# Performance work log

Hardware: AMD Instinct MI355X
Metric: run time of the kernel (lower is better)

The kernel has to match this reference:

```python
import jax, jax.numpy as jnp
import numpy as np

N, E = 20000, 320000
IN_F, H, D = 1280, 4, 128
HD = H * D  # 512
NEG_SLOPE = 0.2


def setup_inputs() -> dict:
    key = jax.random.key(0)
    ks = jax.random.split(key, 16)
    feature = jax.random.normal(ks[0], (1, N, IN_F), dtype=jnp.float32)
    src = jax.random.randint(ks[1], (E,), 0, N, dtype=jnp.int32)
    dst = jnp.sort(jax.random.randint(ks[2], (E,), 0, N, dtype=jnp.int32))
    s1 = 1.0 / np.sqrt(IN_F)
    s2 = 1.0 / np.sqrt(HD)
    W1 = jax.random.normal(ks[3], (IN_F, HD), dtype=jnp.float32) * s1
    al1 = jax.random.normal(ks[4], (H, D), dtype=jnp.float32) * s2
    ar1 = jax.random.normal(ks[5], (H, D), dtype=jnp.float32) * s2
    b1 = jnp.zeros((HD,), dtype=jnp.float32)
    W2 = jax.random.normal(ks[6], (HD, HD), dtype=jnp.float32) * s2
    al2 = jax.random.normal(ks[7], (H, D), dtype=jnp.float32) * s2
    ar2 = jax.random.normal(ks[8], (H, D), dtype=jnp.float32) * s2
    b2 = jnp.zeros((HD,), dtype=jnp.float32)
    Wfc = jax.random.normal(ks[9], (HD, 64), dtype=jnp.float32) * s2
    bfc = jnp.zeros((64,), dtype=jnp.float32)
    return dict(feature=feature, src=src, dst=dst, W1=W1, al1=al1, ar1=ar1,
                b1=b1, W2=W2, al2=al2, ar2=ar2, b2=b2, Wfc=Wfc, bfc=bfc)


def gat_conv(x, src, dst, W, al, ar, b):
    # x: (N, F_in) -> (N, H, D). DGL GATConv math, negative_slope=0.2.
    h = (x @ W).reshape(N, H, D)
    el = jnp.sum(h * al, axis=-1)                       # (N, H)
    er = jnp.sum(h * ar, axis=-1)                       # (N, H)
    e = jax.nn.leaky_relu(el[src] + er[dst], NEG_SLOPE)  # (E, H)
    # edge softmax segmented by destination node
    m = jax.ops.segment_max(e, dst, num_segments=N, indices_are_sorted=True)
    ex = jnp.exp(e - m[dst])                            # (E, H)
    denom = jax.ops.segment_sum(ex, dst, num_segments=N, indices_are_sorted=True)
    alpha = ex / denom[dst]                             # (E, H)
    out = jax.ops.segment_sum(alpha[:, :, None] * h[src], dst,
                              num_segments=N, indices_are_sorted=True)  # (N,H,D)
    return out + b.reshape(H, D)


def reference(feature, src, dst, W1, al1, ar1, b1, W2, al2, ar2, b2, Wfc, bfc):
    x = feature[0]                                      # squeeze(0) -> (N, 1280)
    out = gat_conv(x, src, dst, W1, al1, ar1, b1)
    out = jax.nn.elu(out).reshape(N, HD)
    out = gat_conv(out, src, dst, W2, al2, ar2, b2)
    out = jax.nn.elu(out).reshape(N, HD)
    out = out @ Wfc + bfc                               # (N, 64)
    out = jax.nn.elu(out[None])                         # (1, N, 64)
    return out
```

## Files before the change

### kernel.cpp

```cpp
#include <hip/hip_runtime.h>
#include <hip/hip_bf16.h>
#include <math.h>

typedef __bf16 bf16_t;
typedef __bf16 bf16x8 __attribute__((ext_vector_type(8)));
typedef float f32x4 __attribute__((ext_vector_type(4)));

__device__ __forceinline__ void gload_lds16(const void* g, void* l) {
  __builtin_amdgcn_global_load_lds((const __attribute__((address_space(1))) void*)g,
                                   (__attribute__((address_space(3))) void*)l, 16, 0, 0);
}

__global__ void castk(const float* __restrict__ in, bf16_t* __restrict__ out, int n) {
  int i = (blockIdx.x * blockDim.x + threadIdx.x) * 8;
  if (i >= n) return;
  float4 a = *(const float4*)(in + i);
  float4 b = *(const float4*)(in + i + 4);
  bf16x8 o;
  o[0] = (bf16_t)a.x; o[1] = (bf16_t)a.y; o[2] = (bf16_t)a.z; o[3] = (bf16_t)a.w;
  o[4] = (bf16_t)b.x; o[5] = (bf16_t)b.y; o[6] = (bf16_t)b.z; o[7] = (bf16_t)b.w;
  *(bf16x8*)(out + i) = o;
}

__global__ void transk(const float* __restrict__ in, bf16_t* __restrict__ out,
                       int K, int N) {
  __shared__ float t[32][33];
  int n0 = blockIdx.x * 32, k0 = blockIdx.y * 32;
  int tx = threadIdx.x & 31, ty = threadIdx.x >> 5;
#pragma unroll
  for (int r = ty; r < 32; r += 8) t[r][tx] = in[(size_t)(k0 + r) * N + n0 + tx];
  __syncthreads();
#pragma unroll
  for (int r = ty; r < 32; r += 8)
    out[(size_t)(n0 + r) * K + k0 + tx] = (bf16_t)t[tx][r];
}

__global__ void rowoffk(const int* __restrict__ dst, int* __restrict__ ro, int N, int E) {
  int n = blockIdx.x * blockDim.x + threadIdx.x;
  if (n > N) return;
  if (n == N) { ro[N] = E; return; }
  int lo = 0, hi = E;
  while (lo < hi) { int mid = (lo + hi) >> 1; if (dst[mid] < n) lo = mid + 1; else hi = mid; }
  ro[n] = lo;
}

__global__ void elerk(const bf16_t* __restrict__ Hb, const float* __restrict__ al,
                      const float* __restrict__ ar, float* __restrict__ el,
                      float* __restrict__ er, int N) {
  int node = blockIdx.x * 4 + (threadIdx.x >> 6);
  int lane = threadIdx.x & 63;
  if (node >= N) return;
  bf16x8 v = *(const bf16x8*)(Hb + (size_t)node * 512 + lane * 8);
  int head = lane >> 4;
  int dbase = (lane & 15) * 8;
  float sl = 0.f, sr = 0.f;
#pragma unroll
  for (int t = 0; t < 8; t++) {
    float f = (float)v[t];
    sl += f * al[head * 128 + dbase + t];
    sr += f * ar[head * 128 + dbase + t];
  }
#pragma unroll
  for (int off = 1; off < 16; off <<= 1) {
    sl += __shfl_xor(sl, off);
    sr += __shfl_xor(sr, off);
  }
  if ((lane & 15) == 0) {
    el[node * 4 + head] = sl;
    er[node * 4 + head] = sr;
  }
}

__global__ void edgek(const float* __restrict__ el, const float* __restrict__ er,
                      const int* __restrict__ src, const int* __restrict__ dst,
                      float* __restrict__ pw, int E) {
  int e = blockIdx.x * blockDim.x + threadIdx.x;
  if (e >= E) return;
  int s = src[e], d = dst[e];
  float4 ev = *(const float4*)(el + (size_t)s * 4);
  float4 rv = *(const float4*)(er + (size_t)d * 4);
  float c;
  c = ev.x + rv.x; c = c >= 0.f ? c : 0.2f * c; pw[e] = __expf(c);
  c = ev.y + rv.y; c = c >= 0.f ? c : 0.2f * c; pw[(size_t)E + e] = __expf(c);
  c = ev.z + rv.z; c = c >= 0.f ? c : 0.2f * c; pw[(size_t)2 * E + e] = __expf(c);
  c = ev.w + rv.w; c = c >= 0.f ? c : 0.2f * c; pw[(size_t)3 * E + e] = __expf(c);
}

#define GK_NPB 32
__global__ __launch_bounds__(256) void gatherk(
    const bf16_t* __restrict__ Hb, const float* __restrict__ pw,
    const int* __restrict__ src, const int* __restrict__ ro,
    const float* __restrict__ bias, bf16_t* __restrict__ out, int N, int E) {
  const int slice = blockIdx.x & 7;
  const int group = blockIdx.x >> 3;
  const int w = threadIdx.x >> 6, lane = threadIdx.x & 63;
  const int g = lane >> 3;
  const int oct = lane & 7;
  const int head = slice >> 1;
  const float* __restrict__ ph = pw + (size_t)head * E;
  const int dimbase = slice * 64 + oct * 8;

  const int n = group * GK_NPB + w * 8 + g;
  const int e0 = ro[n], e1 = ro[n + 1];

  float acc[8] = {0.f, 0.f, 0.f, 0.f, 0.f, 0.f, 0.f, 0.f};
  float psum = 0.f;

  for (int e = e0; e < e1; e++) {
    const int s = src[e];
    const float pp = ph[e];
    const bf16x8 v = *(const bf16x8*)(Hb + (size_t)s * 512 + dimbase);
    psum += pp;
#pragma unroll
    for (int t = 0; t < 8; t++) acc[t] += pp * (float)v[t];
  }

  const float ih = psum > 0.f ? 1.0f / psum : 0.f;
  const float4 b0 = *(const float4*)(bias + dimbase);
  const float4 b1 = *(const float4*)(bias + dimbase + 4);
  bf16x8 o; float vv;
  vv = acc[0] * ih + b0.x; o[0] = (bf16_t)(vv > 0.f ? vv : expm1f(vv));
  vv = acc[1] * ih + b0.y; o[1] = (bf16_t)(vv > 0.f ? vv : expm1f(vv));
  vv = acc[2] * ih + b0.z; o[2] = (bf16_t)(vv > 0.f ? vv : expm1f(vv));
  vv = acc[3] * ih + b0.w; o[3] = (bf16_t)(vv > 0.f ? vv : expm1f(vv));
  vv = acc[4] * ih + b1.x; o[4] = (bf16_t)(vv > 0.f ? vv : expm1f(vv));
  vv = acc[5] * ih + b1.y; o[5] = (bf16_t)(vv > 0.f ? vv : expm1f(vv));
  vv = acc[6] * ih + b1.z; o[6] = (bf16_t)(vv > 0.f ? vv : expm1f(vv));
  vv = acc[7] * ih + b1.w; o[7] = (bf16_t)(vv > 0.f ? vv : expm1f(vv));
  *(bf16x8*)(out + (size_t)n * 512 + dimbase) = o;
}

template <int BN, int WM, int WN, int EPI>
__global__ __launch_bounds__(256) void gemm_bt(
    const bf16_t* __restrict__ A, const bf16_t* __restrict__ Bt,
    void* __restrict__ C, const float* __restrict__ bias,
    int M, int N, int K) {
  constexpr int BM = 128, BK = 32;
  constexpr int WTM = BM / WM, WTN = BN / WN;
  constexpr int MF = WTM / 16, NF = WTN / 16;

  __shared__ bf16_t sA[BM][BK];
  __shared__ bf16_t sB[BN][BK];

  const int tid = threadIdx.x;
  const int wid = tid >> 6, lane = tid & 63;
  const int wr = wid / WN, wc = wid % WN;

  const int nby = N / BN;
  const int nwg = gridDim.x;
  const int q = nwg >> 3, r = nwg & 7;
  const int xcd = blockIdx.x & 7, pos = blockIdx.x >> 3;
  const int wg = (xcd < r ? xcd * (q + 1) : r * (q + 1) + (xcd - r) * q) + pos;
  const int row0 = (wg / nby) * BM;
  const int col0 = (wg % nby) * BN;

  f32x4 acc[MF][NF];
#pragma unroll
  for (int i = 0; i < MF; i++)
#pragma unroll
    for (int j = 0; j < NF; j++) acc[i][j] = (f32x4){0.f, 0.f, 0.f, 0.f};

  const int lr = lane >> 2;
  const int lkb = (lane & 3) * 8;

  for (int k0 = 0; k0 < K; k0 += BK) {
#pragma unroll
    for (int i = 0; i < BM / 16; i += 4) {
      int r2 = (i + wid) * 16 + lr;
      int grow = row0 + r2; if (grow > M - 1) grow = M - 1;
      gload_lds16(A + (size_t)grow * K + k0 + lkb, &sA[(i + wid) * 16][0]);
    }
#pragma unroll
    for (int i = 0; i < BN / 16; i += 4) {
      int r2 = (i + wid) * 16 + lr;
      gload_lds16(Bt + (size_t)(col0 + r2) * K + k0 + lkb, &sB[(i + wid) * 16][0]);
    }
    __syncthreads();
    bf16x8 af[MF], bfr[NF];
#pragma unroll
    for (int i = 0; i < MF; i++)
      af[i] = *(const bf16x8*)&sA[wr * WTM + i * 16 + (lane & 15)][(lane >> 4) * 8];
#pragma unroll
    for (int j = 0; j < NF; j++)
      bfr[j] = *(const bf16x8*)&sB[wc * WTN + j * 16 + (lane & 15)][(lane >> 4) * 8];
#pragma unroll
    for (int i = 0; i < MF; i++)
#pragma unroll
      for (int j = 0; j < NF; j++)
        acc[i][j] = __builtin_amdgcn_mfma_f32_16x16x32_bf16(af[i], bfr[j], acc[i][j], 0, 0, 0);
    __syncthreads();
  }

#pragma unroll
  for (int i = 0; i < MF; i++) {
#pragma unroll
    for (int j = 0; j < NF; j++) {
#pragma unroll
      for (int rr = 0; rr < 4; rr++) {
        int row = row0 + wr * WTM + i * 16 + (lane >> 4) * 4 + rr;
        int col = col0 + wc * WTN + j * 16 + (lane & 15);
        if (row < M) {
          float v = acc[i][j][rr];
          if constexpr (EPI == 0) {
            ((bf16_t*)C)[(size_t)row * N + col] = (bf16_t)v;
          } else {
            v += bias[col];
            v = v > 0.f ? v : expm1f(v);
            ((float*)C)[(size_t)row * N + col] = v;
          }
        }
      }
    }
  }
}

extern "C" void kernel_launch(void* const* d_in, const int* in_sizes, int n_in,
                              void* d_out, int out_size, void* d_ws, size_t ws_size,
                              hipStream_t stream) {
  const float* feature = (const float*)d_in[0];
  const int* src = (const int*)d_in[1];
  const int* dst = (const int*)d_in[2];
  const float* W1 = (const float*)d_in[3];
  const float* al1 = (const float*)d_in[4];
  const float* ar1 = (const float*)d_in[5];
  const float* b1 = (const float*)d_in[6];
  const float* W2 = (const float*)d_in[7];
  const float* al2 = (const float*)d_in[8];
  const float* ar2 = (const float*)d_in[9];
  const float* b2 = (const float*)d_in[10];
  const float* Wfc = (const float*)d_in[11];
  const float* bfc = (const float*)d_in[12];

  const int N = 20000, E = 320000, INF = 1280, HD = 512;

  char* ws = (char*)d_ws;
  size_t off = 0;
  auto alloc = [&](size_t bytes) {
    void* p = ws + off;
    off += (bytes + 255) & ~(size_t)255;
    return p;
  };
  bf16_t* Xb  = (bf16_t*)alloc((size_t)N * INF * 2);
  bf16_t* W1t = (bf16_t*)alloc((size_t)HD * INF * 2);
  bf16_t* W2t = (bf16_t*)alloc((size_t)HD * HD * 2);
  bf16_t* Wft = (bf16_t*)alloc((size_t)64 * HD * 2);
  bf16_t* Hb  = (bf16_t*)alloc((size_t)N * HD * 2);
  bf16_t* Xn  = (bf16_t*)alloc((size_t)N * HD * 2);
  float* el = (float*)alloc((size_t)N * 4 * 4);
  float* er = (float*)alloc((size_t)N * 4 * 4);
  float* pw = (float*)alloc((size_t)E * 4 * 4);
  int* ro = (int*)alloc((size_t)(N + 1) * 4);

  castk<<<(N * INF) / (256 * 8), 256, 0, stream>>>(feature, Xb, N * INF);
  {
    dim3 g(HD / 32, INF / 32);
    transk<<<g, 256, 0, stream>>>(W1, W1t, INF, HD);
  }
  {
    dim3 g(HD / 32, HD / 32);
    transk<<<g, 256, 0, stream>>>(W2, W2t, HD, HD);
  }
  {
    dim3 g(64 / 32, HD / 32);
    transk<<<g, 256, 0, stream>>>(Wfc, Wft, HD, 64);
  }
  rowoffk<<<(N + 1 + 255) / 256, 256, 0, stream>>>(dst, ro, N, E);

  const int nbx = (N + 127) / 128;
  const int gatherBlocks = (N / GK_NPB) * 8;
  const int edgeBlocks = (E + 255) / 256;

  gemm_bt<128, 2, 2, 0><<<nbx * (HD / 128), 256, 0, stream>>>(Xb, W1t, Hb, nullptr, N, HD, INF);
  elerk<<<N / 4, 256, 0, stream>>>(Hb, al1, ar1, el, er, N);
  edgek<<<edgeBlocks, 256, 0, stream>>>(el, er, src, dst, pw, E);
  gatherk<<<gatherBlocks, 256, 0, stream>>>(Hb, pw, src, ro, b1, Xn, N, E);

  gemm_bt<128, 2, 2, 0><<<nbx * (HD / 128), 256, 0, stream>>>(Xn, W2t, Hb, nullptr, N, HD, HD);
  elerk<<<N / 4, 256, 0, stream>>>(Hb, al2, ar2, el, er, N);
  edgek<<<edgeBlocks, 256, 0, stream>>>(el, er, src, dst, pw, E);
  gatherk<<<gatherBlocks, 256, 0, stream>>>(Hb, pw, src, ro, b2, Xn, N, E);

  gemm_bt<64, 4, 1, 1><<<nbx, 256, 0, stream>>>(Xn, Wft, d_out, bfc, N, 64, HD);
}
```

Measured before the change: 232.4 us.

## Fuse fp32-to-bf16 feature cast into first GEMM and batch gather edge loads

Removes the separate cast kernel by having the first GEMM read fp32 features directly and convert them to bf16 while staging into LDS. This drops the write and re-read of a bf16 copy of the 20000x1280 input. The change also makes the aggregation gather process edges in aligned groups of eight, with vectorized src and weight loads and eight independent row loads in flight. The fused path gives up the async global-to-LDS load for register round-trips on the A tile. The batched loop does wasted work on masked edges at segment boundaries.

```diff
diff --git a/kernel.cpp b/kernel.cpp
--- a/kernel.cpp
+++ b/kernel.cpp
@@ -9,17 +9,6 @@
 __device__ __forceinline__ void gload_lds16(const void* g, void* l) {
   __builtin_amdgcn_global_load_lds((const __attribute__((address_space(1))) void*)g,
                                    (__attribute__((address_space(3))) void*)l, 16, 0, 0);
-}
-
-__global__ void castk(const float* __restrict__ in, bf16_t* __restrict__ out, int n) {
-  int i = (blockIdx.x * blockDim.x + threadIdx.x) * 8;
-  if (i >= n) return;
-  float4 a = *(const float4*)(in + i);
-  float4 b = *(const float4*)(in + i + 4);
-  bf16x8 o;
-  o[0] = (bf16_t)a.x; o[1] = (bf16_t)a.y; o[2] = (bf16_t)a.z; o[3] = (bf16_t)a.w;
-  o[4] = (bf16_t)b.x; o[5] = (bf16_t)b.y; o[6] = (bf16_t)b.z; o[7] = (bf16_t)b.w;
-  *(bf16x8*)(out + i) = o;
 }
 
 __global__ void transk(const float* __restrict__ in, bf16_t* __restrict__ out,
@@ -106,13 +95,31 @@
   float acc[8] = {0.f, 0.f, 0.f, 0.f, 0.f, 0.f, 0.f, 0.f};
   float psum = 0.f;
 
-  for (int e = e0; e < e1; e++) {
-    const int s = src[e];
-    const float pp = ph[e];
-    const bf16x8 v = *(const bf16x8*)(Hb + (size_t)s * 512 + dimbase);
-    psum += pp;
-#pragma unroll
-    for (int t = 0; t < 8; t++) acc[t] += pp * (float)v[t];
+  for (int eb = e0 & ~7; eb < e1; eb += 8) {
+    const int4 sv0 = *(const int4*)(src + eb);
+    const int4 sv1 = *(const int4*)(src + eb + 4);
+    const float4 pv0 = *(const float4*)(ph + eb);
+    const float4 pv1 = *(const float4*)(ph + eb + 4);
+    int ss[8]; float pp[8];
+    ss[0] = sv0.x; ss[1] = sv0.y; ss[2] = sv0.z; ss[3] = sv0.w;
+    ss[4] = sv1.x; ss[5] = sv1.y; ss[6] = sv1.z; ss[7] = sv1.w;
+    pp[0] = pv0.x; pp[1] = pv0.y; pp[2] = pv0.z; pp[3] = pv0.w;
+    pp[4] = pv1.x; pp[5] = pv1.y; pp[6] = pv1.z; pp[7] = pv1.w;
+#pragma unroll
+    for (int j = 0; j < 8; j++) {
+      const int e = eb + j;
+      if (e < e0 || e >= e1) pp[j] = 0.f;
+    }
+    bf16x8 v[8];
+#pragma unroll
+    for (int j = 0; j < 8; j++)
+      v[j] = *(const bf16x8*)(Hb + (size_t)ss[j] * 512 + dimbase);
+#pragma unroll
+    for (int j = 0; j < 8; j++) {
+      psum += pp[j];
+#pragma unroll
+      for (int t = 0; t < 8; t++) acc[t] += pp[j] * (float)v[j][t];
+    }
   }
 
   const float ih = psum > 0.f ? 1.0f / psum : 0.f;
@@ -130,9 +137,9 @@
   *(bf16x8*)(out + (size_t)n * 512 + dimbase) = o;
 }
 
-template <int BN, int WM, int WN, int EPI>
+template <int BN, int WM, int WN, int EPI, int AF32>
 __global__ __launch_bounds__(256) void gemm_bt(
-    const bf16_t* __restrict__ A, const bf16_t* __restrict__ Bt,
+    const void* __restrict__ A, const bf16_t* __restrict__ Bt,
     void* __restrict__ C, const float* __restrict__ bias,
     int M, int N, int K) {
   constexpr int BM = 128, BK = 32;
@@ -141,6 +148,9 @@
 
   __shared__ bf16_t sA[BM][BK];
   __shared__ bf16_t sB[BN][BK];
+
+  const bf16_t* __restrict__ Ab = (const bf16_t*)A;
+  const float* __restrict__ Af = (const float*)A;
 
   const int tid = threadIdx.x;
   const int wid = tid >> 6, lane = tid & 63;
@@ -162,13 +172,31 @@
 
   const int lr = lane >> 2;
   const int lkb = (lane & 3) * 8;
+  const int arow = tid >> 1;
+  const int ahalf = (tid & 1) * 16;
+  int agrow = row0 + arow; if (agrow > M - 1) agrow = M - 1;
 
   for (int k0 = 0; k0 < K; k0 += BK) {
-#pragma unroll
-    for (int i = 0; i < BM / 16; i += 4) {
-      int r2 = (i + wid) * 16 + lr;
-      int grow = row0 + r2; if (grow > M - 1) grow = M - 1;
-      gload_lds16(A + (size_t)grow * K + k0 + lkb, &sA[(i + wid) * 16][0]);
+    if constexpr (AF32) {
+      const float* ap = Af + (size_t)agrow * K + k0 + ahalf;
+      const float4 f0 = *(const float4*)(ap);
+      const float4 f1 = *(const float4*)(ap + 4);
+      const float4 f2 = *(const float4*)(ap + 8);
+      const float4 f3 = *(const float4*)(ap + 12);
+      bf16x8 w0, w1;
+      w0[0] = (bf16_t)f0.x; w0[1] = (bf16_t)f0.y; w0[2] = (bf16_t)f0.z; w0[3] = (bf16_t)f0.w;
+      w0[4] = (bf16_t)f1.x; w0[5] = (bf16_t)f1.y; w0[6] = (bf16_t)f1.z; w0[7] = (bf16_t)f1.w;
+      w1[0] = (bf16_t)f2.x; w1[1] = (bf16_t)f2.y; w1[2] = (bf16_t)f2.z; w1[3] = (bf16_t)f2.w;
+      w1[4] = (bf16_t)f3.x; w1[5] = (bf16_t)f3.y; w1[6] = (bf16_t)f3.z; w1[7] = (bf16_t)f3.w;
+      *(bf16x8*)&sA[arow][ahalf] = w0;
+      *(bf16x8*)&sA[arow][ahalf + 8] = w1;
+    } else {
+#pragma unroll
+      for (int i = 0; i < BM / 16; i += 4) {
+        int r2 = (i + wid) * 16 + lr;
+        int grow = row0 + r2; if (grow > M - 1) grow = M - 1;
+        gload_lds16(Ab + (size_t)grow * K + k0 + lkb, &sA[(i + wid) * 16][0]);
+      }
     }
 #pragma unroll
     for (int i = 0; i < BN / 16; i += 4) {
@@ -240,7 +268,6 @@
     off += (bytes + 255) & ~(size_t)255;
     return p;
   };
-  bf16_t* Xb  = (bf16_t*)alloc((size_t)N * INF * 2);
   bf16_t* W1t = (bf16_t*)alloc((size_t)HD * INF * 2);
   bf16_t* W2t = (bf16_t*)alloc((size_t)HD * HD * 2);
   bf16_t* Wft = (bf16_t*)alloc((size_t)64 * HD * 2);
@@ -251,7 +278,6 @@
   float* pw = (float*)alloc((size_t)E * 4 * 4);
   int* ro = (int*)alloc((size_t)(N + 1) * 4);
 
-  castk<<<(N * INF) / (256 * 8), 256, 0, stream>>>(feature, Xb, N * INF);
   {
     dim3 g(HD / 32, INF / 32);
     transk<<<g, 256, 0, stream>>>(W1, W1t, INF, HD);
@@ -270,15 +296,15 @@
   const int gatherBlocks = (N / GK_NPB) * 8;
   const int edgeBlocks = (E + 255) / 256;
 
-  gemm_bt<128, 2, 2, 0><<<nbx * (HD / 128), 256, 0, stream>>>(Xb, W1t, Hb, nullptr, N, HD, INF);
+  gemm_bt<128, 2, 2, 0, 1><<<nbx * (HD / 128), 256, 0, stream>>>(feature, W1t, Hb, nullptr, N, HD, INF);
   elerk<<<N / 4, 256, 0, stream>>>(Hb, al1, ar1, el, er, N);
   edgek<<<edgeBlocks, 256, 0, stream>>>(el, er, src, dst, pw, E);
   gatherk<<<gatherBlocks, 256, 0, stream>>>(Hb, pw, src, ro, b1, Xn, N, E);
 
-  gemm_bt<128, 2, 2, 0><<<nbx * (HD / 128), 256, 0, stream>>>(Xn, W2t, Hb, nullptr, N, HD, HD);
+  gemm_bt<128, 2, 2, 0, 0><<<nbx * (HD / 128), 256, 0, stream>>>(Xn, W2t, Hb, nullptr, N, HD, HD);
   elerk<<<N / 4, 256, 0, stream>>>(Hb, al2, ar2, el, er, N);
   edgek<<<edgeBlocks, 256, 0, stream>>>(el, er, src, dst, pw, E);
   gatherk<<<gatherBlocks, 256, 0, stream>>>(Hb, pw, src, ro, b2, Xn, N, E);
 
-  gemm_bt<64, 4, 1, 1><<<nbx, 256, 0, stream>>>(Xn, Wft, d_out, bfc, N, 64, HD);
-}
+  gemm_bt<64, 4, 1, 1, 0><<<nbx, 256, 0, stream>>>(Xn, Wft, d_out, bfc, N, 64, HD);
+}
```

New measurement: 218.5 us. 6.0% less time.

## Batch gather edge loads by eight and shrink GEMM tiles for more blocks

Applied to the files above, without the earlier changes.

The gather kernel now loads src indices and weights eight at a time with vector loads and issues eight independent row loads before accumulating. Edges outside the node's range are masked by zeroing their weights. This raises memory-level parallelism in the latency-bound gather. The GEMMs now take BM as a template parameter and use smaller 128x64 and 64x64 tiles, which launch more workgroups on the 256-CU device at the cost of less data reuse per tile. Aligning the start down to a multiple of eight may read src/pw slightly past e1 near the end of the arrays, which is a possible out-of-bounds risk.

```diff
diff --git a/kernel.cpp b/kernel.cpp
--- a/kernel.cpp
+++ b/kernel.cpp
@@ -106,13 +106,31 @@
   float acc[8] = {0.f, 0.f, 0.f, 0.f, 0.f, 0.f, 0.f, 0.f};
   float psum = 0.f;
 
-  for (int e = e0; e < e1; e++) {
-    const int s = src[e];
-    const float pp = ph[e];
-    const bf16x8 v = *(const bf16x8*)(Hb + (size_t)s * 512 + dimbase);
-    psum += pp;
-#pragma unroll
-    for (int t = 0; t < 8; t++) acc[t] += pp * (float)v[t];
+  for (int eb = e0 & ~7; eb < e1; eb += 8) {
+    const int4 sv0 = *(const int4*)(src + eb);
+    const int4 sv1 = *(const int4*)(src + eb + 4);
+    const float4 pv0 = *(const float4*)(ph + eb);
+    const float4 pv1 = *(const float4*)(ph + eb + 4);
+    int ss[8]; float pp[8];
+    ss[0] = sv0.x; ss[1] = sv0.y; ss[2] = sv0.z; ss[3] = sv0.w;
+    ss[4] = sv1.x; ss[5] = sv1.y; ss[6] = sv1.z; ss[7] = sv1.w;
+    pp[0] = pv0.x; pp[1] = pv0.y; pp[2] = pv0.z; pp[3] = pv0.w;
+    pp[4] = pv1.x; pp[5] = pv1.y; pp[6] = pv1.z; pp[7] = pv1.w;
+#pragma unroll
+    for (int j = 0; j < 8; j++) {
+      const int e = eb + j;
+      if (e < e0 || e >= e1) pp[j] = 0.f;
+    }
+    bf16x8 v[8];
+#pragma unroll
+    for (int j = 0; j < 8; j++)
+      v[j] = *(const bf16x8*)(Hb + (size_t)ss[j] * 512 + dimbase);
+#pragma unroll
+    for (int j = 0; j < 8; j++) {
+      psum += pp[j];
+#pragma unroll
+      for (int t = 0; t < 8; t++) acc[t] += pp[j] * (float)v[j][t];
+    }
   }
 
   const float ih = psum > 0.f ? 1.0f / psum : 0.f;
@@ -130,12 +148,12 @@
   *(bf16x8*)(out + (size_t)n * 512 + dimbase) = o;
 }
 
-template <int BN, int WM, int WN, int EPI>
+template <int BM, int BN, int WM, int WN, int EPI>
 __global__ __launch_bounds__(256) void gemm_bt(
     const bf16_t* __restrict__ A, const bf16_t* __restrict__ Bt,
     void* __restrict__ C, const float* __restrict__ bias,
     int M, int N, int K) {
-  constexpr int BM = 128, BK = 32;
+  constexpr int BK = 32;
   constexpr int WTM = BM / WM, WTN = BN / WN;
   constexpr int MF = WTM / 16, NF = WTN / 16;
 
@@ -267,18 +285,19 @@
   rowoffk<<<(N + 1 + 255) / 256, 256, 0, stream>>>(dst, ro, N, E);
 
   const int nbx = (N + 127) / 128;
+  const int nbxf = (N + 63) / 64;
   const int gatherBlocks = (N / GK_NPB) * 8;
   const int edgeBlocks = (E + 255) / 256;
 
-  gemm_bt<128, 2, 2, 0><<<nbx * (HD / 128), 256, 0, stream>>>(Xb, W1t, Hb, nullptr, N, HD, INF);
+  gemm_bt<128, 64, 2, 2, 0><<<nbx * (HD / 64), 256, 0, stream>>>(Xb, W1t, Hb, nullptr, N, HD, INF);
   elerk<<<N / 4, 256, 0, stream>>>(Hb, al1, ar1, el, er, N);
   edgek<<<edgeBlocks, 256, 0, stream>>>(el, er, src, dst, pw, E);
   gatherk<<<gatherBlocks, 256, 0, stream>>>(Hb, pw, src, ro, b1, Xn, N, E);
 
-  gemm_bt<128, 2, 2, 0><<<nbx * (HD / 128), 256, 0, stream>>>(Xn, W2t, Hb, nullptr, N, HD, HD);
+  gemm_bt<128, 64, 2, 2, 0><<<nbx * (HD / 64), 256, 0, stream>>>(Xn, W2t, Hb, nullptr, N, HD, HD);
   elerk<<<N / 4, 256, 0, stream>>>(Hb, al2, ar2, el, er, N);
   edgek<<<edgeBlocks, 256, 0, stream>>>(el, er, src, dst, pw, E);
   gatherk<<<gatherBlocks, 256, 0, stream>>>(Hb, pw, src, ro, b2, Xn, N, E);
 
-  gemm_bt<64, 4, 1, 1><<<nbx, 256, 0, stream>>>(Xn, Wft, d_out, bfc, N, 64, HD);
-}
+  gemm_bt<64, 64, 2, 2, 1><<<nbxf, 256, 0, stream>>>(Xn, Wft, d_out, bfc, N, 64, HD);
+}
```

Measured after the change: 214.0 us. 1.09x faster.
